# Kernel optimization log

Hardware: AMD Instinct MI355X
Metric: run time of the kernel (lower is better)

Reference implementation:

```python
import jax, jax.numpy as jnp
import numpy as np

D_MODEL = 512
N_HEADS = 8
D_K = 64
D_V = 64
FACTOR = 1  # Autoformer AutoCorrelation default


def setup_inputs() -> dict:
    key = jax.random.key(0)
    ks = jax.random.split(key, 7)
    B, L = 8, 2048
    Q = jax.random.normal(ks[0], (B, L, D_MODEL), dtype=jnp.float32)
    K = jax.random.normal(ks[1], (B, L, D_MODEL), dtype=jnp.float32)
    V = jax.random.normal(ks[2], (B, L, D_MODEL), dtype=jnp.float32)
    s = 1.0 / np.sqrt(D_MODEL)
    WQ = jax.random.normal(ks[3], (D_MODEL, N_HEADS * D_K), dtype=jnp.float32) * s
    WK = jax.random.normal(ks[4], (D_MODEL, N_HEADS * D_K), dtype=jnp.float32) * s
    WV = jax.random.normal(ks[5], (D_MODEL, N_HEADS * D_V), dtype=jnp.float32) * s
    Wfc = jax.random.normal(ks[6], (N_HEADS * D_V, D_MODEL), dtype=jnp.float32) * s
    return {"Q": Q, "K": K, "V": V, "WQ": WQ, "WK": WK, "WV": WV, "Wfc": Wfc}


def _autocorrelation(q, k, v):
    # q, k, v: [B, L, H, E] (Autoformer AutoCorrelation, training-mode agg)
    B, L, H, E = q.shape
    qf = jnp.fft.rfft(q.transpose(0, 2, 3, 1), axis=-1)  # [B,H,E,Lf]
    kf = jnp.fft.rfft(k.transpose(0, 2, 3, 1), axis=-1)
    corr = jnp.fft.irfft(qf * jnp.conj(kf), n=L, axis=-1)  # [B,H,E,L]
    vals = v.transpose(0, 2, 3, 1)  # [B,H,E,L]
    top_k = int(FACTOR * np.log(L))
    mean_value = corr.mean(axis=(1, 2))  # [B,L] mean over heads & channels
    _, index = jax.lax.top_k(mean_value.mean(axis=0), top_k)  # [top_k] shared delays
    weights = mean_value[:, index]  # [B, top_k]
    tmp_corr = jax.nn.softmax(weights, axis=-1)  # [B, top_k]
    # roll(vals, -index[i]) along time for each selected delay, fully vectorized
    gather_idx = (jnp.arange(L)[None, :] + index[:, None]) % L  # [top_k, L]
    rolled = vals[..., gather_idx]  # [B,H,E,top_k,L]
    agg = jnp.einsum('bhekl,bk->bhel', rolled, tmp_corr)  # [B,H,E,L]
    return agg.transpose(0, 3, 1, 2)  # [B,L,H,E]


def reference(Q, K, V, WQ, WK, WV, Wfc):
    B, L, _ = Q.shape
    q_s = (Q @ WQ).reshape(B, L, N_HEADS, D_K)
    k_s = (K @ WK).reshape(B, L, N_HEADS, D_K)
    v_s = (V @ WV).reshape(B, L, N_HEADS, D_V)
    context = _autocorrelation(q_s, k_s, v_s)  # [B,L,H,Dv]
    context = context.reshape(B, L, N_HEADS * D_V)
    return context @ Wfc  # [B,L,d_model]
```

## Files before the change

kernel.cpp:

```cpp
#include <hip/hip_runtime.h>
#include <math.h>

#define B_ 8
#define L_ 2048
#define D_ 512
#define LOG2L 11
#define TOPK 7
#define M_ (B_ * L_)

typedef __attribute__((ext_vector_type(8))) _Float16 half8;
typedef __attribute__((ext_vector_type(4))) _Float16 half4;
typedef __attribute__((ext_vector_type(4))) float f32x4;

__global__ __launch_bounds__(256) void convw_kernel(
    const float* __restrict__ W0, const float* __restrict__ W1,
    const float* __restrict__ W2, const float* __restrict__ W3,
    _Float16* __restrict__ T0, _Float16* __restrict__ T1,
    _Float16* __restrict__ T2, _Float16* __restrict__ T3)
{
  __shared__ float tile[64][65];
  const int t = (int)threadIdx.x;
  const int mat = (int)blockIdx.x >> 6;
  const int tb = (int)blockIdx.x & 63;
  const float* W = (mat == 0) ? W0 : (mat == 1) ? W1 : (mat == 2) ? W2 : W3;
  _Float16* Wt = (mat == 0) ? T0 : (mat == 1) ? T1 : (mat == 2) ? T2 : T3;
  const int k0 = (tb >> 3) * 64;
  const int n0 = (tb & 7) * 64;
#pragma unroll
  for (int i = 0; i < 4; ++i) {
    const int kl = (t >> 4) + i * 16;
    const float4 v = *reinterpret_cast<const float4*>(&W[(size_t)(k0 + kl) * D_ + n0 + (t & 15) * 4]);
    tile[kl][(t & 15) * 4 + 0] = v.x;
    tile[kl][(t & 15) * 4 + 1] = v.y;
    tile[kl][(t & 15) * 4 + 2] = v.z;
    tile[kl][(t & 15) * 4 + 3] = v.w;
  }
  __syncthreads();
  const int nl = t >> 2, q = t & 3;
  half8 h0, h1;
#pragma unroll
  for (int j = 0; j < 8; ++j) {
    h0[j] = (_Float16)tile[q * 16 + j][nl];
    h1[j] = (_Float16)tile[q * 16 + 8 + j][nl];
  }
  _Float16* dst = &Wt[(size_t)(n0 + nl) * D_ + k0 + q * 16];
  *reinterpret_cast<half8*>(dst) = h0;
  *reinterpret_cast<half8*>(dst + 8) = h1;
}

#define LDSTR 40
#define NWG 1024

template <int INBF, int OUTMODE>
__global__ __launch_bounds__(256) void gemm_f16_kernel(
    const float* __restrict__ Af, const _Float16* __restrict__ Ah,
    const _Float16* __restrict__ Wt,
    float* __restrict__ Cf, _Float16* __restrict__ Ch)
{
  __shared__ __align__(16) _Float16 sA[64 * LDSTR];
  __shared__ __align__(16) _Float16 sB[128 * LDSTR];

  const int bid = (int)blockIdx.x;
  const int wg = (bid & 7) * (NWG >> 3) + (bid >> 3);
  const int m0 = (wg >> 2) << 6;
  const int n0 = (wg & 3) << 7;

  const int tid = (int)threadIdx.x;
  const int lane = tid & 63, wave = tid >> 6;
  const int wr = (wave >> 1) << 5;
  const int wc = (wave & 1) << 6;

  const int arow = tid >> 2;
  const int ac0 = (tid & 3) << 3;
  const int brow = tid >> 1;
  const int bc0 = (tid & 1) << 4;

  f32x4 acc[2][4];
  const f32x4 zero = {0.f, 0.f, 0.f, 0.f};
#pragma unroll
  for (int i = 0; i < 2; ++i)
#pragma unroll
    for (int j = 0; j < 4; ++j) acc[i][j] = zero;

  const int fr = lane & 15;
  const int g8 = (lane >> 4) << 3;

  for (int k0 = 0; k0 < D_; k0 += 32) {
    half8 ha, hb0, hb1;
    if constexpr (INBF == 0) {
      const float* ap = Af + (size_t)(m0 + arow) * D_ + k0 + ac0;
      const float4 v0 = *reinterpret_cast<const float4*>(ap);
      const float4 v1 = *reinterpret_cast<const float4*>(ap + 4);
      ha[0] = (_Float16)v0.x; ha[1] = (_Float16)v0.y;
      ha[2] = (_Float16)v0.z; ha[3] = (_Float16)v0.w;
      ha[4] = (_Float16)v1.x; ha[5] = (_Float16)v1.y;
      ha[6] = (_Float16)v1.z; ha[7] = (_Float16)v1.w;
    } else {
      ha = *reinterpret_cast<const half8*>(Ah + (size_t)(m0 + arow) * D_ + k0 + ac0);
    }
    {
      const _Float16* bp = Wt + (size_t)(n0 + brow) * D_ + k0 + bc0;
      hb0 = *reinterpret_cast<const half8*>(bp);
      hb1 = *reinterpret_cast<const half8*>(bp + 8);
    }

    __syncthreads();
    *reinterpret_cast<half8*>(&sA[arow * LDSTR + ac0]) = ha;
    *reinterpret_cast<half8*>(&sB[brow * LDSTR + bc0]) = hb0;
    *reinterpret_cast<half8*>(&sB[brow * LDSTR + bc0 + 8]) = hb1;
    __syncthreads();

    half8 afr[2], bfr[4];
#pragma unroll
    for (int i = 0; i < 2; ++i)
      afr[i] = *reinterpret_cast<const half8*>(&sA[(wr + i * 16 + fr) * LDSTR + g8]);
#pragma unroll
    for (int i = 0; i < 4; ++i)
      bfr[i] = *reinterpret_cast<const half8*>(&sB[(wc + i * 16 + fr) * LDSTR + g8]);
#pragma unroll
    for (int mi = 0; mi < 2; ++mi)
#pragma unroll
      for (int ni = 0; ni < 4; ++ni)
        acc[mi][ni] = __builtin_amdgcn_mfma_f32_16x16x32_f16(afr[mi], bfr[ni], acc[mi][ni], 0, 0, 0);
  }

  const int orow = (lane >> 4) << 2;
  const int ocol = lane & 15;
  if constexpr (OUTMODE == 0) {
#pragma unroll
    for (int mi = 0; mi < 2; ++mi)
#pragma unroll
      for (int ni = 0; ni < 4; ++ni)
#pragma unroll
        for (int r = 0; r < 4; ++r)
          Cf[(size_t)(m0 + wr + mi * 16 + orow + r) * D_ + n0 + wc + ni * 16 + ocol] = acc[mi][ni][r];
  } else if constexpr (OUTMODE == 2) {
#pragma unroll
    for (int mi = 0; mi < 2; ++mi)
#pragma unroll
      for (int ni = 0; ni < 4; ++ni)
#pragma unroll
        for (int r = 0; r < 4; ++r)
          Ch[(size_t)(m0 + wr + mi * 16 + orow + r) * D_ + n0 + wc + ni * 16 + ocol] = (_Float16)acc[mi][ni][r];
  } else {
#pragma unroll
    for (int ni = 0; ni < 4; ++ni) {
      const size_t nrow = (size_t)(n0 + wc + ni * 16 + ocol) * M_;
#pragma unroll
      for (int mi = 0; mi < 2; ++mi) {
        half4 hv;
        hv[0] = (_Float16)acc[mi][ni][0]; hv[1] = (_Float16)acc[mi][ni][1];
        hv[2] = (_Float16)acc[mi][ni][2]; hv[3] = (_Float16)acc[mi][ni][3];
        *reinterpret_cast<half4*>(&Ch[nrow + m0 + wr + mi * 16 + orow]) = hv;
      }
    }
  }
}

__device__ __forceinline__ int rev11(int x) {
  return (int)(__brev((unsigned)x) >> (32 - LOG2L));
}

#define DCHUNK 4
#define PADI(i) ((i) + ((i) >> 5))

#define BFLY(j0, j1, wr_, wi_) { \
  const float ar = xr[j0], ai = xi[j0], br = xr[j1], bi = xi[j1]; \
  xr[j0] = ar + br; xi[j0] = ai + bi; \
  const float tr = ar - br, ti = ai - bi; \
  xr[j1] = tr * (wr_) - ti * (wi_); \
  xi[j1] = tr * (wi_) + ti * (wr_); }

__global__ __launch_bounds__(256) void corr_fft_kernel(
    const _Float16* __restrict__ qT, const _Float16* __restrict__ kT,
    float* __restrict__ S)
{
  __shared__ float re[2112];
  __shared__ float im[2112];
  const int t = (int)threadIdx.x;
  const int blk = (int)blockIdx.x;
  const int b = blk >> 7;
  const int d0 = (blk & 127) * DCHUNK;
  const int u2 = t & 31, u3 = t & 3;

  float w2048r, w2048i, w256r, w256i, w32r, w32i;
  {
    float s_, c_;
    __sincosf(-6.283185307179586f * (float)t / 2048.f, &s_, &c_);
    w2048r = c_; w2048i = s_;
    __sincosf(-6.283185307179586f * (float)u2 / 256.f, &s_, &c_);
    w256r = c_; w256i = s_;
    __sincosf(-6.283185307179586f * (float)u3 / 32.f, &s_, &c_);
    w32r = c_; w32i = s_;
  }
  const float w1024r = w2048r * w2048r - w2048i * w2048i, w1024i = 2.f * w2048r * w2048i;
  const float w512r  = w1024r * w1024r - w1024i * w1024i, w512i  = 2.f * w1024r * w1024i;
  const float w128r  = w256r * w256r - w256i * w256i,     w128i  = 2.f * w256r * w256i;
  const float w64r   = w128r * w128r - w128i * w128i,     w64i   = 2.f * w128r * w128i;
  const float w16r   = w32r * w32r - w32i * w32i,         w16i   = 2.f * w32r * w32i;
  const float w8r    = w16r * w16r - w16i * w16i,         w8i    = 2.f * w16r * w16i;

  const float C_ = 0.70710678118654752f;
  const float W8R[4] = {1.f, C_, 0.f, -C_};
  const float W8I[4] = {0.f, -C_, -1.f, -C_};

  float pr[8] = {}, pi_[8] = {};

  for (int dc = 0; dc < DCHUNK; ++dc) {
    const int d = d0 + dc;
    const _Float16* qrow = qT + (size_t)d * M_ + (size_t)b * L_;
    const _Float16* krow = kT + (size_t)d * M_ + (size_t)b * L_;

    float xr[8], xi[8];
#pragma unroll
    for (int j = 0; j < 8; ++j) {
      xr[j] = (float)qrow[t + 256 * j];
      xi[j] = (float)krow[t + 256 * j];
    }

#pragma unroll
    for (int j = 0; j < 4; ++j) {
      const float wr_ = w2048r * W8R[j] - w2048i * W8I[j];
      const float wi_ = w2048r * W8I[j] + w2048i * W8R[j];
      BFLY(j, j + 4, wr_, wi_);
    }
#pragma unroll
    for (int base = 0; base < 8; base += 4) {
      BFLY(base + 0, base + 2, w1024r, w1024i);
      BFLY(base + 1, base + 3, w1024i, -w1024r);
    }
#pragma unroll
    for (int a = 0; a < 8; a += 2) BFLY(a, a + 1, w512r, w512i);

    __syncthreads();
#pragma unroll
    for (int j = 0; j < 8; ++j) {
      const int p = t + 256 * j;
      re[PADI(p)] = xr[j]; im[PADI(p)] = xi[j];
    }
    __syncthreads();
#pragma unroll
    for (int j = 0; j < 8; ++j) {
      const int p = ((t >> 5) << 8) + u2 + 32 * j;
      xr[j] = re[PADI(p)]; xi[j] = im[PADI(p)];
    }

#pragma unroll
    for (int j = 0; j < 4; ++j) {
      const float wr_ = w256r * W8R[j] - w256i * W8I[j];
      const float wi_ = w256r * W8I[j] + w256i * W8R[j];
      BFLY(j, j + 4, wr_, wi_);
    }
#pragma unroll
    for (int base = 0; base < 8; base += 4) {
      BFLY(base + 0, base + 2, w128r, w128i);
      BFLY(base + 1, base + 3, w128i, -w128r);
    }
#pragma unroll
    for (int a = 0; a < 8; a += 2) BFLY(a, a + 1, w64r, w64i);

    __syncthreads();
#pragma unroll
    for (int j = 0; j < 8; ++j) {
      const int p = ((t >> 5) << 8) + u2 + 32 * j;
      re[PADI(p)] = xr[j]; im[PADI(p)] = xi[j];
    }
    __syncthreads();
#pragma unroll
    for (int j = 0; j < 8; ++j) {
      const int p = ((t >> 2) << 5) + u3 + 4 * j;
      xr[j] = re[PADI(p)]; xi[j] = im[PADI(p)];
    }

#pragma unroll
    for (int j = 0; j < 4; ++j) {
      const float wr_ = w32r * W8R[j] - w32i * W8I[j];
      const float wi_ = w32r * W8I[j] + w32i * W8R[j];
      BFLY(j, j + 4, wr_, wi_);
    }
#pragma unroll
    for (int base = 0; base < 8; base += 4) {
      BFLY(base + 0, base + 2, w16r, w16i);
      BFLY(base + 1, base + 3, w16i, -w16r);
    }
#pragma unroll
    for (int a = 0; a < 8; a += 2) BFLY(a, a + 1, w8r, w8i);

    __syncthreads();
#pragma unroll
    for (int j = 0; j < 8; ++j) {
      const int p = ((t >> 2) << 5) + u3 + 4 * j;
      re[PADI(p)] = xr[j]; im[PADI(p)] = xi[j];
    }
    __syncthreads();
#pragma unroll
    for (int j = 0; j < 8; ++j) {
      const int p = 8 * t + j;
      xr[j] = re[PADI(p)]; xi[j] = im[PADI(p)];
    }

#pragma unroll
    for (int base = 0; base < 8; base += 4) {
      BFLY(base + 0, base + 2, 1.f, 0.f);
      BFLY(base + 1, base + 3, 0.f, -1.f);
    }
#pragma unroll
    for (int a = 0; a < 8; a += 2) BFLY(a, a + 1, 1.f, 0.f);

#pragma unroll
    for (int j = 0; j < 8; ++j) {
      const int p = 8 * t + j;
      re[PADI(p)] = xr[j]; im[PADI(p)] = xi[j];
    }
    __syncthreads();

#pragma unroll
    for (int i = 0; i < 8; ++i) {
      const int p = t + 256 * i;
      const int f = rev11(p);
      const int fm = (L_ - f) & (L_ - 1);
      const int pm = rev11(fm);
      const float Ar = re[PADI(p)],  Ai = im[PADI(p)];
      const float Br = re[PADI(pm)], Bi = -im[PADI(pm)];
      const float Qr = 0.5f * (Ar + Br), Qi = 0.5f * (Ai + Bi);
      const float Cr = 0.5f * (Ai - Bi), Ci = 0.5f * (Ar - Br);
      pr[i]  += Qr * Cr - Qi * Ci;
      pi_[i] += Qr * Ci + Qi * Cr;
    }
    if (dc + 1 < DCHUNK) __syncthreads();
  }

#pragma unroll
  for (int i = 0; i < 8; ++i) {
    const int p = t + 256 * i;
    const int f = rev11(p);
    if (f <= L_ / 2) {
      atomicAdd(&S[((size_t)b * L_ + p) * 2 + 0], pr[i]);
      atomicAdd(&S[((size_t)b * L_ + p) * 2 + 1], pi_[i]);
    }
  }
}

__global__ __launch_bounds__(256) void ifft_kernel(
    const float* __restrict__ S, float* __restrict__ mv)
{
  __shared__ float re[L_];
  __shared__ float im[L_];
  const int b = blockIdx.x;
  for (int p = (int)threadIdx.x; p < L_; p += 256) {
    const int f = rev11(p);
    float sr, si;
    if (f <= L_ / 2) {
      sr = S[((size_t)b * L_ + p) * 2 + 0];
      si = S[((size_t)b * L_ + p) * 2 + 1];
    } else {
      const int pm = rev11(L_ - f);
      sr = S[((size_t)b * L_ + pm) * 2 + 0];
      si = -S[((size_t)b * L_ + pm) * 2 + 1];
    }
    re[p] = sr; im[p] = si;
  }
  __syncthreads();
  for (int s = 1; s <= LOG2L; ++s) {
    const int half = 1 << (s - 1);
    for (int j = (int)threadIdx.x; j < (L_ >> 1); j += 256) {
      const int pos = j & (half - 1);
      const int i0 = ((j >> (s - 1)) << s) + pos;
      const int i1 = i0 + half;
      const float ang = 3.14159265358979323846f * (float)pos / (float)half;
      float wi, wr;
      __sincosf(ang, &wi, &wr);
      const float br = re[i1], bi = im[i1];
      const float tr = br * wr - bi * wi;
      const float ti = br * wi + bi * wr;
      const float ar = re[i0], ai = im[i0];
      re[i0] = ar + tr; im[i0] = ai + ti;
      re[i1] = ar - tr; im[i1] = ai - ti;
    }
    __syncthreads();
  }
  const float scale = 1.0f / ((float)D_ * (float)L_);
  for (int l = (int)threadIdx.x; l < L_; l += 256)
    mv[(size_t)b * L_ + l] = re[l] * scale;
}

__global__ __launch_bounds__(1024) void topk_kernel(
    const float* __restrict__ mv, int* __restrict__ idx, float* __restrict__ wts)
{
  __shared__ float vals[L_];
  __shared__ float wm[16];
  __shared__ int wi[16];
  __shared__ int chosen[TOPK];
  const int t = (int)threadIdx.x;
  const int lane = t & 63, wv = t >> 6;
  float s0 = 0.f, s1 = 0.f;
#pragma unroll
  for (int b = 0; b < B_; ++b) {
    s0 += mv[(size_t)b * L_ + t];
    s1 += mv[(size_t)b * L_ + t + 1024];
  }
  vals[t] = s0; vals[t + 1024] = s1;
  __syncthreads();
  for (int kk = 0; kk < TOPK; ++kk) {
    float v0 = vals[t]; int i0 = t;
    const float v1 = vals[t + 1024];
    if (v1 > v0) { v0 = v1; i0 = t + 1024; }
#pragma unroll
    for (int off = 32; off; off >>= 1) {
      const float ov = __shfl_xor(v0, off, 64);
      const int oi = __shfl_xor(i0, off, 64);
      if (ov > v0 || (ov == v0 && oi < i0)) { v0 = ov; i0 = oi; }
    }
    if (lane == 0) { wm[wv] = v0; wi[wv] = i0; }
    __syncthreads();
    if (t == 0) {
      float m = wm[0]; int mi = wi[0];
      for (int i2 = 1; i2 < 16; ++i2)
        if (wm[i2] > m || (wm[i2] == m && wi[i2] < mi)) { m = wm[i2]; mi = wi[i2]; }
      chosen[kk] = mi; idx[kk] = mi; vals[mi] = -1e30f;
    }
    __syncthreads();
  }
  if (t < B_) {
    float w[TOPK];
    float mx = -1e30f;
#pragma unroll
    for (int kk = 0; kk < TOPK; ++kk) {
      w[kk] = mv[(size_t)t * L_ + chosen[kk]];
      mx = fmaxf(mx, w[kk]);
    }
    float sum = 0.f;
#pragma unroll
    for (int kk = 0; kk < TOPK; ++kk) { w[kk] = __expf(w[kk] - mx); sum += w[kk]; }
    const float inv = 1.0f / sum;
#pragma unroll
    for (int kk = 0; kk < TOPK; ++kk) wts[t * TOPK + kk] = w[kk] * inv;
  }
}

__global__ __launch_bounds__(256) void context_kernel(
    const _Float16* __restrict__ v, const int* __restrict__ idx,
    const float* __restrict__ wts, _Float16* __restrict__ ctx)
{
  const int raw = (int)blockIdx.x;
  const int wg = (raw & 7) * 512 + (raw >> 3);
  const int b = wg >> 9;
  const int l = ((wg & 511) << 2) + ((int)threadIdx.x >> 6);
  const int lane = (int)threadIdx.x & 63;
  float acc[8] = {};
#pragma unroll
  for (int kk = 0; kk < TOPK; ++kk) {
    const float w = wts[b * TOPK + kk];
    const int src = (l + idx[kk]) & (L_ - 1);
    const half8 x = *reinterpret_cast<const half8*>(v + ((size_t)(b << LOG2L) + src) * D_ + lane * 8);
#pragma unroll
    for (int j = 0; j < 8; ++j) acc[j] = fmaf(w, (float)x[j], acc[j]);
  }
  half8 o;
#pragma unroll
  for (int j = 0; j < 8; ++j) o[j] = (_Float16)acc[j];
  *reinterpret_cast<half8*>(ctx + ((size_t)(b << LOG2L) + l) * D_ + lane * 8) = o;
}

extern "C" void kernel_launch(void* const* d_in, const int* in_sizes, int n_in,
                              void* d_out, int out_size, void* d_ws, size_t ws_size,
                              hipStream_t stream)
{
  (void)in_sizes; (void)n_in; (void)out_size; (void)ws_size;
  const float* Q   = (const float*)d_in[0];
  const float* K   = (const float*)d_in[1];
  const float* V   = (const float*)d_in[2];
  const float* WQ  = (const float*)d_in[3];
  const float* WK  = (const float*)d_in[4];
  const float* WV  = (const float*)d_in[5];
  const float* Wfc = (const float*)d_in[6];
  float* out = (float*)d_out;

  char* ws = (char*)d_ws;
  const size_t sz_h   = (size_t)M_ * D_ * sizeof(_Float16);
  const size_t sz_w16 = (size_t)D_ * D_ * sizeof(_Float16);
  _Float16*  qT16  = (_Float16*)(ws);
  _Float16*  kT16  = (_Float16*)(ws + sz_h);
  _Float16*  vs16  = (_Float16*)(ws + 2 * sz_h);
  _Float16*  ctx16 = (_Float16*)(ws + 3 * sz_h);
  _Float16*  WQt   = (_Float16*)(ws + 4 * sz_h);
  _Float16*  WKt   = (_Float16*)(ws + 4 * sz_h + sz_w16);
  _Float16*  WVt   = (_Float16*)(ws + 4 * sz_h + 2 * sz_w16);
  _Float16*  Wfct  = (_Float16*)(ws + 4 * sz_h + 3 * sz_w16);
  float*     S     = (float*)(ws + 4 * sz_h + 4 * sz_w16);
  float*     mv    = (float*)((char*)S + (size_t)B_ * L_ * 2 * sizeof(float));
  int*       idx   = (int*)((char*)mv + (size_t)B_ * L_ * sizeof(float));
  float*     wts   = (float*)((char*)idx + 64);

  convw_kernel<<<256, 256, 0, stream>>>(WQ, WK, WV, Wfc, WQt, WKt, WVt, Wfct);
  hipMemsetAsync(S, 0, (size_t)B_ * L_ * 2 * sizeof(float), stream);

  gemm_f16_kernel<0, 3><<<NWG, 256, 0, stream>>>(Q, nullptr, WQt, nullptr, qT16);
  gemm_f16_kernel<0, 3><<<NWG, 256, 0, stream>>>(K, nullptr, WKt, nullptr, kT16);

  corr_fft_kernel<<<B_ * (D_ / DCHUNK), 256, 0, stream>>>(qT16, kT16, S);
  ifft_kernel<<<B_, 256, 0, stream>>>(S, mv);
  topk_kernel<<<1, 1024, 0, stream>>>(mv, idx, wts);

  gemm_f16_kernel<0, 2><<<NWG, 256, 0, stream>>>(V, nullptr, WVt, nullptr, vs16);
  context_kernel<<<4096, 256, 0, stream>>>(vs16, idx, wts, ctx16);
  gemm_f16_kernel<1, 0><<<NWG, 256, 0, stream>>>(nullptr, ctx16, Wfct, out, nullptr);
}
```

Measured before the change: 177.1 us.

## Double GEMM K-tile, ping-pong FFT LDS buffers, widen ifft to 1024 threads

The GEMM now stages a 64-wide K slice per iteration instead of 32, halving barrier and loop overhead at the cost of more LDS and registers. The correlation FFT alternates between two shared-memory buffers so the write-after-read barriers before each transpose can be removed, which doubles its LDS footprint. The inverse FFT kernel launches 1024 threads so each does a single butterfly per stage instead of looping.

```diff
diff --git a/kernel.cpp b/kernel.cpp
--- a/kernel.cpp
+++ b/kernel.cpp
@@ -48,7 +48,7 @@
   *reinterpret_cast<half8*>(dst + 8) = h1;
 }
 
-#define LDSTR 40
+#define LDSTR 72
 #define NWG 1024
 
 template <int INBF, int OUTMODE>
@@ -71,9 +71,9 @@
   const int wc = (wave & 1) << 6;
 
   const int arow = tid >> 2;
-  const int ac0 = (tid & 3) << 3;
+  const int ac0 = (tid & 3) << 4;
   const int brow = tid >> 1;
-  const int bc0 = (tid & 1) << 4;
+  const int bc0 = (tid & 1) << 5;
 
   f32x4 acc[2][4];
   const f32x4 zero = {0.f, 0.f, 0.f, 0.f};
@@ -85,43 +85,56 @@
   const int fr = lane & 15;
   const int g8 = (lane >> 4) << 3;
 
-  for (int k0 = 0; k0 < D_; k0 += 32) {
-    half8 ha, hb0, hb1;
+  for (int k0 = 0; k0 < D_; k0 += 64) {
+    half8 ha0, ha1, hb0, hb1, hb2, hb3;
     if constexpr (INBF == 0) {
       const float* ap = Af + (size_t)(m0 + arow) * D_ + k0 + ac0;
-      const float4 v0 = *reinterpret_cast<const float4*>(ap);
-      const float4 v1 = *reinterpret_cast<const float4*>(ap + 4);
-      ha[0] = (_Float16)v0.x; ha[1] = (_Float16)v0.y;
-      ha[2] = (_Float16)v0.z; ha[3] = (_Float16)v0.w;
-      ha[4] = (_Float16)v1.x; ha[5] = (_Float16)v1.y;
-      ha[6] = (_Float16)v1.z; ha[7] = (_Float16)v1.w;
+      float tmp[16];
+#pragma unroll
+      for (int j = 0; j < 4; ++j) {
+        const float4 v = *reinterpret_cast<const float4*>(ap + j * 4);
+        tmp[j * 4 + 0] = v.x; tmp[j * 4 + 1] = v.y;
+        tmp[j * 4 + 2] = v.z; tmp[j * 4 + 3] = v.w;
+      }
+#pragma unroll
+      for (int j = 0; j < 8; ++j) { ha0[j] = (_Float16)tmp[j]; ha1[j] = (_Float16)tmp[8 + j]; }
     } else {
-      ha = *reinterpret_cast<const half8*>(Ah + (size_t)(m0 + arow) * D_ + k0 + ac0);
+      const _Float16* ap = Ah + (size_t)(m0 + arow) * D_ + k0 + ac0;
+      ha0 = *reinterpret_cast<const half8*>(ap);
+      ha1 = *reinterpret_cast<const half8*>(ap + 8);
     }
     {
       const _Float16* bp = Wt + (size_t)(n0 + brow) * D_ + k0 + bc0;
       hb0 = *reinterpret_cast<const half8*>(bp);
       hb1 = *reinterpret_cast<const half8*>(bp + 8);
-    }
-
-    __syncthreads();
-    *reinterpret_cast<half8*>(&sA[arow * LDSTR + ac0]) = ha;
+      hb2 = *reinterpret_cast<const half8*>(bp + 16);
+      hb3 = *reinterpret_cast<const half8*>(bp + 24);
+    }
+
+    __syncthreads();
+    *reinterpret_cast<half8*>(&sA[arow * LDSTR + ac0]) = ha0;
+    *reinterpret_cast<half8*>(&sA[arow * LDSTR + ac0 + 8]) = ha1;
     *reinterpret_cast<half8*>(&sB[brow * LDSTR + bc0]) = hb0;
     *reinterpret_cast<half8*>(&sB[brow * LDSTR + bc0 + 8]) = hb1;
-    __syncthreads();
-
-    half8 afr[2], bfr[4];
-#pragma unroll
-    for (int i = 0; i < 2; ++i)
-      afr[i] = *reinterpret_cast<const half8*>(&sA[(wr + i * 16 + fr) * LDSTR + g8]);
-#pragma unroll
-    for (int i = 0; i < 4; ++i)
-      bfr[i] = *reinterpret_cast<const half8*>(&sB[(wc + i * 16 + fr) * LDSTR + g8]);
-#pragma unroll
-    for (int mi = 0; mi < 2; ++mi)
-#pragma unroll
-      for (int ni = 0; ni < 4; ++ni)
-        acc[mi][ni] = __builtin_amdgcn_mfma_f32_16x16x32_f16(afr[mi], bfr[ni], acc[mi][ni], 0, 0, 0);
+    *reinterpret_cast<half8*>(&sB[brow * LDSTR + bc0 + 16]) = hb2;
+    *reinterpret_cast<half8*>(&sB[brow * LDSTR + bc0 + 24]) = hb3;
+    __syncthreads();
+
+#pragma unroll
+    for (int ks = 0; ks < 64; ks += 32) {
+      half8 afr[2], bfr[4];
+#pragma unroll
+      for (int i = 0; i < 2; ++i)
+        afr[i] = *reinterpret_cast<const half8*>(&sA[(wr + i * 16 + fr) * LDSTR + ks + g8]);
+#pragma unroll
+      for (int i = 0; i < 4; ++i)
+        bfr[i] = *reinterpret_cast<const half8*>(&sB[(wc + i * 16 + fr) * LDSTR + ks + g8]);
+#pragma unroll
+      for (int mi = 0; mi < 2; ++mi)
+#pragma unroll
+        for (int ni = 0; ni < 4; ++ni)
+          acc[mi][ni] = __builtin_amdgcn_mfma_f32_16x16x32_f16(afr[mi], bfr[ni], acc[mi][ni], 0, 0, 0);
+    }
   }
 
   const int orow = (lane >> 4) << 2;
@@ -175,8 +188,8 @@
     const _Float16* __restrict__ qT, const _Float16* __restrict__ kT,
     float* __restrict__ S)
 {
-  __shared__ float re[2112];
-  __shared__ float im[2112];
+  __shared__ float re0[2112], im0[2112];
+  __shared__ float re1[2112], im1[2112];
   const int t = (int)threadIdx.x;
   const int blk = (int)blockIdx.x;
   const int b = blk >> 7;
@@ -232,17 +245,16 @@
 #pragma unroll
     for (int a = 0; a < 8; a += 2) BFLY(a, a + 1, w512r, w512i);
 
-    __syncthreads();
 #pragma unroll
     for (int j = 0; j < 8; ++j) {
       const int p = t + 256 * j;
-      re[PADI(p)] = xr[j]; im[PADI(p)] = xi[j];
+      re0[PADI(p)] = xr[j]; im0[PADI(p)] = xi[j];
     }
     __syncthreads();
 #pragma unroll
     for (int j = 0; j < 8; ++j) {
       const int p = ((t >> 5) << 8) + u2 + 32 * j;
-      xr[j] = re[PADI(p)]; xi[j] = im[PADI(p)];
+      xr[j] = re0[PADI(p)]; xi[j] = im0[PADI(p)];
     }
 
 #pragma unroll
@@ -259,17 +271,16 @@
 #pragma unroll
     for (int a = 0; a < 8; a += 2) BFLY(a, a + 1, w64r, w64i);
 
-    __syncthreads();
 #pragma unroll
     for (int j = 0; j < 8; ++j) {
       const int p = ((t >> 5) << 8) + u2 + 32 * j;
-      re[PADI(p)] = xr[j]; im[PADI(p)] = xi[j];
+      re1[PADI(p)] = xr[j]; im1[PADI(p)] = xi[j];
     }
     __syncthreads();
 #pragma unroll
     for (int j = 0; j < 8; ++j) {
       const int p = ((t >> 2) << 5) + u3 + 4 * j;
-      xr[j] = re[PADI(p)]; xi[j] = im[PADI(p)];
+      xr[j] = re1[PADI(p)]; xi[j] = im1[PADI(p)];
     }
 
 #pragma unroll
@@ -286,17 +297,16 @@
 #pragma unroll
     for (int a = 0; a < 8; a += 2) BFLY(a, a + 1, w8r, w8i);
 
-    __syncthreads();
 #pragma unroll
     for (int j = 0; j < 8; ++j) {
       const int p = ((t >> 2) << 5) + u3 + 4 * j;
-      re[PADI(p)] = xr[j]; im[PADI(p)] = xi[j];
+      re0[PADI(p)] = xr[j]; im0[PADI(p)] = xi[j];
     }
     __syncthreads();
 #pragma unroll
     for (int j = 0; j < 8; ++j) {
       const int p = 8 * t + j;
-      xr[j] = re[PADI(p)]; xi[j] = im[PADI(p)];
+      xr[j] = re0[PADI(p)]; xi[j] = im0[PADI(p)];
     }
 
 #pragma unroll
@@ -310,7 +320,7 @@
 #pragma unroll
     for (int j = 0; j < 8; ++j) {
       const int p = 8 * t + j;
-      re[PADI(p)] = xr[j]; im[PADI(p)] = xi[j];
+      re1[PADI(p)] = xr[j]; im1[PADI(p)] = xi[j];
     }
     __syncthreads();
 
@@ -320,14 +330,13 @@
       const int f = rev11(p);
       const int fm = (L_ - f) & (L_ - 1);
       const int pm = rev11(fm);
-      const float Ar = re[PADI(p)],  Ai = im[PADI(p)];
-      const float Br = re[PADI(pm)], Bi = -im[PADI(pm)];
+      const float Ar = re1[PADI(p)],  Ai = im1[PADI(p)];
+      const float Br = re1[PADI(pm)], Bi = -im1[PADI(pm)];
       const float Qr = 0.5f * (Ar + Br), Qi = 0.5f * (Ai + Bi);
       const float Cr = 0.5f * (Ai - Bi), Ci = 0.5f * (Ar - Br);
       pr[i]  += Qr * Cr - Qi * Ci;
       pi_[i] += Qr * Ci + Qi * Cr;
     }
-    if (dc + 1 < DCHUNK) __syncthreads();
   }
 
 #pragma unroll
@@ -341,13 +350,13 @@
   }
 }
 
-__global__ __launch_bounds__(256) void ifft_kernel(
+__global__ __launch_bounds__(1024) void ifft_kernel(
     const float* __restrict__ S, float* __restrict__ mv)
 {
   __shared__ float re[L_];
   __shared__ float im[L_];
   const int b = blockIdx.x;
-  for (int p = (int)threadIdx.x; p < L_; p += 256) {
+  for (int p = (int)threadIdx.x; p < L_; p += 1024) {
     const int f = rev11(p);
     float sr, si;
     if (f <= L_ / 2) {
@@ -363,7 +372,8 @@
   __syncthreads();
   for (int s = 1; s <= LOG2L; ++s) {
     const int half = 1 << (s - 1);
-    for (int j = (int)threadIdx.x; j < (L_ >> 1); j += 256) {
+    {
+      const int j = (int)threadIdx.x;
       const int pos = j & (half - 1);
       const int i0 = ((j >> (s - 1)) << s) + pos;
       const int i1 = i0 + half;
@@ -380,7 +390,7 @@
     __syncthreads();
   }
   const float scale = 1.0f / ((float)D_ * (float)L_);
-  for (int l = (int)threadIdx.x; l < L_; l += 256)
+  for (int l = (int)threadIdx.x; l < L_; l += 1024)
     mv[(size_t)b * L_ + l] = re[l] * scale;
 }
 
@@ -499,7 +509,7 @@
   gemm_f16_kernel<0, 3><<<NWG, 256, 0, stream>>>(K, nullptr, WKt, nullptr, kT16);
 
   corr_fft_kernel<<<B_ * (D_ / DCHUNK), 256, 0, stream>>>(qT16, kT16, S);
-  ifft_kernel<<<B_, 256, 0, stream>>>(S, mv);
+  ifft_kernel<<<B_, 1024, 0, stream>>>(S, mv);
   topk_kernel<<<1, 1024, 0, stream>>>(mv, idx, wts);
 
   gemm_f16_kernel<0, 2><<<NWG, 256, 0, stream>>>(V, nullptr, WVt, nullptr, vs16);
```

After: 173.9 us. Within noise of the previous version (-1.8%).
